# Optimization experiments

Hardware: AMD Instinct MI355X
Metric: run time of the kernel (lower is better)

The kernel has to match this reference:

```python
import jax, jax.numpy as jnp
import numpy as np

INPUT_SIZE = 64
HIDDEN = 128
BATCH = 512
SEQ = 512


def setup_inputs() -> dict:
    key = jax.random.key(0)
    ks = jax.random.split(key, 7)
    s_ih = 1.0 / np.sqrt(HIDDEN)
    token = jax.random.normal(ks[0], (BATCH, SEQ, INPUT_SIZE), dtype=jnp.float32)
    W_ih = jax.random.uniform(ks[1], (HIDDEN, INPUT_SIZE), jnp.float32, -s_ih, s_ih)
    W_hh = jax.random.uniform(ks[2], (HIDDEN, HIDDEN), jnp.float32, -s_ih, s_ih)
    b_ih = jax.random.uniform(ks[3], (HIDDEN,), jnp.float32, -s_ih, s_ih)
    b_hh = jax.random.uniform(ks[4], (HIDDEN,), jnp.float32, -s_ih, s_ih)
    W_lin = jax.random.uniform(ks[5], (1, HIDDEN), jnp.float32, -s_ih, s_ih)
    b_lin = jax.random.uniform(ks[6], (1,), jnp.float32, -s_ih, s_ih)
    return {"token": token, "W_ih": W_ih, "W_hh": W_hh, "b_ih": b_ih,
            "b_hh": b_hh, "W_lin": W_lin, "b_lin": b_lin}


def reference(token, W_ih, W_hh, b_ih, b_hh, W_lin, b_lin):
    # Precompute input projection for all timesteps: [T, B, H]
    x_proj = jnp.einsum('bti,hi->tbh', token, W_ih) + b_ih + b_hh
    h0 = jnp.zeros((token.shape[0], W_hh.shape[0]), dtype=token.dtype)

    def step(h, xp):
        h_new = jnp.tanh(xp + h @ W_hh.T)
        return h_new, None

    h_last, _ = jax.lax.scan(step, h0, x_proj)
    # Linear head on last hidden state: [B, 1]
    return h_last @ W_lin.T + b_lin
```

## Files before the change

kernel.cpp:

```cpp
#include <hip/hip_runtime.h>

#define B_ 512
#define T_ 512
#define I_ 64
#define H_ 128
#define CHUNK 64
#define NCHUNK (T_ / CHUNK)

#define TOKBYTES 16384
#define HB0      (2 * TOKBYTES)
#define HB1      (HB0 + 512)
#define DUMMY    (HB1 + 512)
#define LDS_SZ   (DUMMY + 256)

__device__ __forceinline__ void gload_lds16(const float* g, void* l) {
    __builtin_amdgcn_global_load_lds(
        (const __attribute__((address_space(1))) unsigned int*)g,
        (__attribute__((address_space(3))) unsigned int*)l, 16, 0, 0);
}

#define FM(a, x, w) "v_fmac_f32 v" #a ", v" #x ", v" #w "\n\t"
#define SC(n) "v_mul_f32 v" #n ", 0x4038aa3b, v" #n "\n\t"

#define CLOBS \
    "v48","v49","v50","v51","v52","v53","v54","v55","v56","v57","v58","v59", \
    "v60","v61","v62","v63","v64","v65","v66","v67","v68","v69","v70","v71", \
    "v72","v73","v74","v75","v76","v77","v78","v79","v80","v81","v82","v83", \
    "v84","v85","v86","v87","v88","v89","v90","v91","v92","v93","v94","v95", \
    "v96","v97","v98","v99","v100","v101","v102","v103","v104","v105","v106", \
    "v107","v108","v109","v110","v111","v112","v113","v114","v115","v116", \
    "v117","v118","v119","v120","v121","v122","v123","v124","v125","v126", \
    "v127","memory"

#define RNN_STEP(TOKA, HRD, HWR, BA, BB, PAR)                                 \
    asm volatile(                                                             \
        "ds_read_b128 v[56:59], %0\n\t"                                       \
        "ds_read_b128 v[60:63], %0 offset:128\n\t"                            \
        "ds_read_b128 v[64:67], %1\n\t"                                       \
        "ds_read_b128 v[68:71], %1 offset:128\n\t"                            \
        "ds_read_b128 v[72:75], %1 offset:256\n\t"                            \
        "ds_read_b128 v[76:79], %1 offset:384\n\t"                            \
        "v_add_u32 %0, 256, %0\n\t"                                           \
        "s_waitcnt lgkmcnt(4)\n\t"                                            \
        "v_fma_f32 v48, v56, v112, %3\n\t"                                    \
        "v_mul_f32 v49, v57, v113\n\t"                                        \
        "v_mul_f32 v50, v58, v114\n\t"                                        \
        "v_mul_f32 v51, v59, v115\n\t"                                        \
        "v_fma_f32 v52, v56, v120, %4\n\t"                                    \
        "v_mul_f32 v53, v57, v121\n\t"                                        \
        "v_mul_f32 v54, v58, v122\n\t"                                        \
        "v_mul_f32 v55, v59, v123\n\t"                                        \
        FM(48,60,116) FM(49,61,117) FM(50,62,118) FM(51,63,119)               \
        FM(52,60,124) FM(53,61,125) FM(54,62,126) FM(55,63,127)               \
        "s_waitcnt lgkmcnt(2)\n\t"                                            \
        FM(48,64,80)  FM(49,65,81)  FM(50,66,82)  FM(51,67,83)                \
        FM(52,64,96)  FM(53,65,97)  FM(54,66,98)  FM(55,67,99)                \
        FM(48,68,84)  FM(49,69,85)  FM(50,70,86)  FM(51,71,87)                \
        FM(52,68,100) FM(53,69,101) FM(54,70,102) FM(55,71,103)               \
        "s_waitcnt lgkmcnt(0)\n\t"                                            \
        FM(48,72,88)  FM(49,73,89)  FM(50,74,90)  FM(51,75,91)                \
        FM(52,72,104) FM(53,73,105) FM(54,74,106) FM(55,75,107)               \
        FM(48,76,92)  FM(49,77,93)  FM(50,78,94)  FM(51,79,95)                \
        FM(52,76,108) FM(53,77,109) FM(54,78,110) FM(55,79,111)               \
        "v_add_f32 v48, v48, v49\n\t"                                         \
        "v_add_f32 v50, v50, v51\n\t"                                         \
        "v_add_f32 v52, v52, v53\n\t"                                         \
        "v_add_f32 v54, v54, v55\n\t"                                         \
        "v_add_f32 v48, v48, v50\n\t"                                         \
        "v_add_f32 v52, v52, v54\n\t"                                         \
        "s_nop 1\n\t"                                                         \
        "v_add_f32 v48, v48, v48 quad_perm:[1,0,3,2] row_mask:0xf bank_mask:0xf\n\t" \
        "v_add_f32 v52, v52, v52 quad_perm:[1,0,3,2] row_mask:0xf bank_mask:0xf\n\t" \
        "v_cndmask_b32 v49, v48, v52, %5\n\t"                                 \
        "s_nop 1\n\t"                                                         \
        "v_add_f32 v49, v49, v49 quad_perm:[2,3,0,1] row_mask:0xf bank_mask:0xf\n\t" \
        "s_nop 1\n\t"                                                         \
        "v_add_f32 v49, v49, v49 row_shl:4 row_mask:0xf bank_mask:0x5\n\t"    \
        "s_nop 1\n\t"                                                         \
        "v_exp_f32 v49, v49\n\t"                                              \
        "s_nop 0\n\t"                                                         \
        "v_add_f32 v49, 1.0, v49\n\t"                                         \
        "v_rcp_f32 v50, v49\n\t"                                              \
        "s_nop 0\n\t"                                                         \
        "v_fma_f32 v49, v50, -2.0, 1.0\n\t"                                   \
        "ds_write_b32 %2, v49\n\t"                                            \
        "s_waitcnt lgkmcnt(0)\n\t"                                            \
        "s_barrier"                                                           \
        : "+v"(TOKA)                                                          \
        : "v"(HRD), "v"(HWR), "v"(BA), "v"(BB), "s"(PAR)                      \
        : CLOBS)

__global__ __launch_bounds__(512) __attribute__((amdgpu_waves_per_eu(4, 4)))
void rnn_kernel(const float* __restrict__ token,
                const float* __restrict__ W_ih,
                const float* __restrict__ W_hh,
                const float* __restrict__ b_ih,
                const float* __restrict__ b_hh,
                const float* __restrict__ W_lin,
                const float* __restrict__ b_lin,
                float* __restrict__ out)
{
    __shared__ __align__(16) char lds[LDS_SZ];
    const unsigned lb =
        (unsigned)(uintptr_t)(__attribute__((address_space(3))) char*)lds;

    const int tid = threadIdx.x;
    const int e   = tid & 7;
    const int G   = tid >> 3;
    const int b   = blockIdx.x;
    const int j0  = 2 * G, j1 = 2 * G + 1;

    {
        const float* pA = W_hh + j0 * H_ + e * 16;
        const float* pB = W_hh + j1 * H_ + e * 16;
        const float* pC = W_ih + j0 * I_ + e * 8;
        const float* pD = W_ih + j1 * I_ + e * 8;
        asm volatile(
            "global_load_dwordx4 v[80:83], %0, off\n\t"
            "global_load_dwordx4 v[84:87], %0, off offset:16\n\t"
            "global_load_dwordx4 v[88:91], %0, off offset:32\n\t"
            "global_load_dwordx4 v[92:95], %0, off offset:48\n\t"
            "global_load_dwordx4 v[96:99], %1, off\n\t"
            "global_load_dwordx4 v[100:103], %1, off offset:16\n\t"
            "global_load_dwordx4 v[104:107], %1, off offset:32\n\t"
            "global_load_dwordx4 v[108:111], %1, off offset:48\n\t"
            "global_load_dwordx4 v[112:115], %2, off\n\t"
            "global_load_dwordx4 v[116:119], %2, off offset:16\n\t"
            "global_load_dwordx4 v[120:123], %3, off\n\t"
            "global_load_dwordx4 v[124:127], %3, off offset:16\n\t"
            "s_waitcnt vmcnt(0)\n\t"
            SC(80) SC(81) SC(82) SC(83) SC(84) SC(85) SC(86) SC(87)
            SC(88) SC(89) SC(90) SC(91) SC(92) SC(93) SC(94) SC(95)
            SC(96) SC(97) SC(98) SC(99) SC(100) SC(101) SC(102) SC(103)
            SC(104) SC(105) SC(106) SC(107) SC(108) SC(109) SC(110) SC(111)
            SC(112) SC(113) SC(114) SC(115) SC(116) SC(117) SC(118) SC(119)
            SC(120) SC(121) SC(122) SC(123) SC(124) SC(125) SC(126) SC(127)
            :: "v"(pA), "v"(pB), "v"(pC), "v"(pD) : CLOBS);
    }

    const float biasA = (b_ih[j0] + b_hh[j0]) * (2.885390081777927f / 8.0f);
    const float biasB = (b_ih[j1] + b_hh[j1]) * (2.885390081777927f / 8.0f);
    const unsigned long long par = 0xAAAAAAAAAAAAAAAAULL;

    const int  jsel   = 2 * G + (e & 1);
    const int  wloc   = ((jsel >> 2) & 3) * 32 + (jsel >> 4) * 4 + (jsel & 3);
    const bool writer = (e < 2);
    const unsigned dmy = lb + DUMMY + (tid & 63) * 4;
    const unsigned hw0 = writer ? (lb + HB1 + wloc * 4) : dmy;
    const unsigned hw1 = writer ? (lb + HB0 + wloc * 4) : dmy;
    const unsigned hr0 = lb + HB0 + e * 16;
    const unsigned hr1 = lb + HB1 + e * 16;

    const float* tok_row = token + (size_t)b * T_ * I_;
    const int S0 = tid, S1 = 512 + tid;
    const int so0 = (S0 >> 4) * 64 + (S0 & 7) * 8 + ((S0 >> 3) & 1) * 4;
    const int so1 = (S1 >> 4) * 64 + (S1 & 7) * 8 + ((S1 >> 3) & 1) * 4;

    gload_lds16(tok_row + so0, lds + S0 * 16);
    gload_lds16(tok_row + so1, lds + S1 * 16);
    if (tid < H_) *(float*)(lds + HB0 + tid * 4) = 0.0f;
    asm volatile("s_waitcnt vmcnt(0) lgkmcnt(0)\n\ts_barrier" ::: "memory");

#pragma unroll 1
    for (int c = 0; c < NCHUNK; ++c) {
        const int cb = c & 1;
        const bool has_next = (c + 1 < NCHUNK);
        if (has_next) {
            const float* g = tok_row + (size_t)(c + 1) * CHUNK * I_;
            char* dst = lds + (cb ^ 1) * TOKBYTES;
            gload_lds16(g + so0, dst + S0 * 16);
            gload_lds16(g + so1, dst + S1 * 16);
        }
        unsigned toka = lb + cb * TOKBYTES + e * 16;

#pragma unroll 1
        for (int tt = 0; tt < CHUNK; tt += 2) {
            RNN_STEP(toka, hr0, hw0, biasA, biasB, par);
            RNN_STEP(toka, hr1, hw1, biasA, biasB, par);
        }

        if (has_next) {
            asm volatile("s_waitcnt vmcnt(0)\n\ts_barrier" ::: "memory");
        }
    }

    if (tid < 64) {
        const int a0 = tid, a1 = tid + 64;
        const int l0 = ((a0 >> 2) & 3) * 32 + (a0 >> 4) * 4 + (a0 & 3);
        const int l1 = ((a1 >> 2) & 3) * 32 + (a1 >> 4) * 4 + (a1 & 3);
        float p = *(const float*)(lds + HB0 + l0 * 4) * W_lin[a0]
                + *(const float*)(lds + HB0 + l1 * 4) * W_lin[a1];
#pragma unroll
        for (int off = 32; off; off >>= 1) p += __shfl_down(p, off);
        if (tid == 0) out[b] = p + b_lin[0];
    }
}

extern "C" void kernel_launch(void* const* d_in, const int* in_sizes, int n_in,
                              void* d_out, int out_size, void* d_ws, size_t ws_size,
                              hipStream_t stream) {
    const float* token = (const float*)d_in[0];
    const float* W_ih  = (const float*)d_in[1];
    const float* W_hh  = (const float*)d_in[2];
    const float* b_ih  = (const float*)d_in[3];
    const float* b_hh  = (const float*)d_in[4];
    const float* W_lin = (const float*)d_in[5];
    const float* b_lin = (const float*)d_in[6];
    float* out = (float*)d_out;

    hipLaunchKernelGGL(rnn_kernel, dim3(B_), dim3(512), 0, stream,
                       token, W_ih, W_hh, b_ih, b_hh, W_lin, b_lin, out);
}
```

Measured before the change: 230.3 us.

## Split each hidden row across 16 lanes with 4 rows per group

Work is redistributed so each group of 16 lanes computes 4 hidden units instead of 8 lanes computing 2. Each lane now reads fewer LDS vectors per step (3 b128 instead of 6) and drops the partial-sum add tree, relying on a DPP butterfly with two select masks to merge four outputs. The goal is to shorten the per-step critical path in the serial recurrence. The token and hidden-state LDS layouts and the writer-address mapping change to match, with the risk of a longer cross-lane reduction chain.

```diff
diff --git a/kernel.cpp b/kernel.cpp
--- a/kernel.cpp
+++ b/kernel.cpp
@@ -32,62 +32,58 @@
     "v117","v118","v119","v120","v121","v122","v123","v124","v125","v126", \
     "v127","memory"
 
-#define RNN_STEP(TOKA, HRD, HWR, BA, BB, PAR)                                 \
+#define RNN_STEP(TOKA, HRD, HWR, BA, BB, BC, BD, M1, M2)                      \
     asm volatile(                                                             \
         "ds_read_b128 v[56:59], %0\n\t"                                       \
-        "ds_read_b128 v[60:63], %0 offset:128\n\t"                            \
         "ds_read_b128 v[64:67], %1\n\t"                                       \
-        "ds_read_b128 v[68:71], %1 offset:128\n\t"                            \
-        "ds_read_b128 v[72:75], %1 offset:256\n\t"                            \
-        "ds_read_b128 v[76:79], %1 offset:384\n\t"                            \
+        "ds_read_b128 v[68:71], %1 offset:256\n\t"                            \
         "v_add_u32 %0, 256, %0\n\t"                                           \
-        "s_waitcnt lgkmcnt(4)\n\t"                                            \
+        "s_waitcnt lgkmcnt(2)\n\t"                                            \
         "v_fma_f32 v48, v56, v112, %3\n\t"                                    \
-        "v_mul_f32 v49, v57, v113\n\t"                                        \
-        "v_mul_f32 v50, v58, v114\n\t"                                        \
-        "v_mul_f32 v51, v59, v115\n\t"                                        \
-        "v_fma_f32 v52, v56, v120, %4\n\t"                                    \
-        "v_mul_f32 v53, v57, v121\n\t"                                        \
-        "v_mul_f32 v54, v58, v122\n\t"                                        \
-        "v_mul_f32 v55, v59, v123\n\t"                                        \
-        FM(48,60,116) FM(49,61,117) FM(50,62,118) FM(51,63,119)               \
-        FM(52,60,124) FM(53,61,125) FM(54,62,126) FM(55,63,127)               \
-        "s_waitcnt lgkmcnt(2)\n\t"                                            \
-        FM(48,64,80)  FM(49,65,81)  FM(50,66,82)  FM(51,67,83)                \
-        FM(52,64,96)  FM(53,65,97)  FM(54,66,98)  FM(55,67,99)                \
-        FM(48,68,84)  FM(49,69,85)  FM(50,70,86)  FM(51,71,87)                \
-        FM(52,68,100) FM(53,69,101) FM(54,70,102) FM(55,71,103)               \
+        "v_fma_f32 v49, v56, v116, %4\n\t"                                    \
+        "v_fma_f32 v50, v56, v120, %5\n\t"                                    \
+        "v_fma_f32 v51, v56, v124, %6\n\t"                                    \
+        FM(48,57,113) FM(49,57,117) FM(50,57,121) FM(51,57,125)               \
+        FM(48,58,114) FM(49,58,118) FM(50,58,122) FM(51,58,126)               \
+        FM(48,59,115) FM(49,59,119) FM(50,59,123) FM(51,59,127)               \
+        "s_waitcnt lgkmcnt(1)\n\t"                                            \
+        FM(48,64,80) FM(49,64,88) FM(50,64,96)  FM(51,64,104)                 \
+        FM(48,65,81) FM(49,65,89) FM(50,65,97)  FM(51,65,105)                 \
+        FM(48,66,82) FM(49,66,90) FM(50,66,98)  FM(51,66,106)                 \
+        FM(48,67,83) FM(49,67,91) FM(50,67,99)  FM(51,67,107)                 \
         "s_waitcnt lgkmcnt(0)\n\t"                                            \
-        FM(48,72,88)  FM(49,73,89)  FM(50,74,90)  FM(51,75,91)                \
-        FM(52,72,104) FM(53,73,105) FM(54,74,106) FM(55,75,107)               \
-        FM(48,76,92)  FM(49,77,93)  FM(50,78,94)  FM(51,79,95)                \
-        FM(52,76,108) FM(53,77,109) FM(54,78,110) FM(55,79,111)               \
-        "v_add_f32 v48, v48, v49\n\t"                                         \
-        "v_add_f32 v50, v50, v51\n\t"                                         \
-        "v_add_f32 v52, v52, v53\n\t"                                         \
-        "v_add_f32 v54, v54, v55\n\t"                                         \
-        "v_add_f32 v48, v48, v50\n\t"                                         \
-        "v_add_f32 v52, v52, v54\n\t"                                         \
+        FM(48,68,84) FM(49,68,92) FM(50,68,100) FM(51,68,108)                 \
+        FM(48,69,85) FM(49,69,93) FM(50,69,101) FM(51,69,109)                 \
+        FM(48,70,86) FM(49,70,94) FM(50,70,102) FM(51,70,110)                 \
+        FM(48,71,87) FM(49,71,95) FM(50,71,103) FM(51,71,111)                 \
         "s_nop 1\n\t"                                                         \
         "v_add_f32 v48, v48, v48 quad_perm:[1,0,3,2] row_mask:0xf bank_mask:0xf\n\t" \
-        "v_add_f32 v52, v52, v52 quad_perm:[1,0,3,2] row_mask:0xf bank_mask:0xf\n\t" \
-        "v_cndmask_b32 v49, v48, v52, %5\n\t"                                 \
-        "s_nop 1\n\t"                                                         \
-        "v_add_f32 v49, v49, v49 quad_perm:[2,3,0,1] row_mask:0xf bank_mask:0xf\n\t" \
-        "s_nop 1\n\t"                                                         \
-        "v_add_f32 v49, v49, v49 row_shl:4 row_mask:0xf bank_mask:0x5\n\t"    \
-        "s_nop 1\n\t"                                                         \
-        "v_exp_f32 v49, v49\n\t"                                              \
+        "v_add_f32 v49, v49, v49 quad_perm:[1,0,3,2] row_mask:0xf bank_mask:0xf\n\t" \
+        "v_add_f32 v50, v50, v50 quad_perm:[1,0,3,2] row_mask:0xf bank_mask:0xf\n\t" \
+        "v_add_f32 v51, v51, v51 quad_perm:[1,0,3,2] row_mask:0xf bank_mask:0xf\n\t" \
+        "v_cndmask_b32 v52, v48, v49, %7\n\t"                                 \
+        "v_cndmask_b32 v53, v50, v51, %7\n\t"                                 \
         "s_nop 0\n\t"                                                         \
-        "v_add_f32 v49, 1.0, v49\n\t"                                         \
-        "v_rcp_f32 v50, v49\n\t"                                              \
+        "v_add_f32 v52, v52, v52 quad_perm:[2,3,0,1] row_mask:0xf bank_mask:0xf\n\t" \
+        "v_add_f32 v53, v53, v53 quad_perm:[2,3,0,1] row_mask:0xf bank_mask:0xf\n\t" \
+        "v_cndmask_b32 v54, v52, v53, %8\n\t"                                 \
+        "s_nop 1\n\t"                                                         \
+        "v_add_f32 v54, v54, v54 row_shl:8 row_mask:0xf bank_mask:0x3\n\t"    \
+        "s_nop 1\n\t"                                                         \
+        "v_add_f32 v54, v54, v54 row_shl:4 row_mask:0xf bank_mask:0x1\n\t"    \
+        "s_nop 1\n\t"                                                         \
+        "v_exp_f32 v54, v54\n\t"                                              \
         "s_nop 0\n\t"                                                         \
-        "v_fma_f32 v49, v50, -2.0, 1.0\n\t"                                   \
-        "ds_write_b32 %2, v49\n\t"                                            \
+        "v_add_f32 v54, 1.0, v54\n\t"                                         \
+        "v_rcp_f32 v55, v54\n\t"                                              \
+        "s_nop 0\n\t"                                                         \
+        "v_fma_f32 v54, v55, -2.0, 1.0\n\t"                                   \
+        "ds_write_b32 %2, v54\n\t"                                            \
         "s_waitcnt lgkmcnt(0)\n\t"                                            \
         "s_barrier"                                                           \
         : "+v"(TOKA)                                                          \
-        : "v"(HRD), "v"(HWR), "v"(BA), "v"(BB), "s"(PAR)                      \
+        : "v"(HRD), "v"(HWR), "v"(BA), "v"(BB), "v"(BC), "v"(BD),             \
+          "s"(M1), "s"(M2)                                                    \
         : CLOBS)
 
 __global__ __launch_bounds__(512) __attribute__((amdgpu_waves_per_eu(4, 4)))
@@ -105,29 +101,27 @@
         (unsigned)(uintptr_t)(__attribute__((address_space(3))) char*)lds;
 
     const int tid = threadIdx.x;
-    const int e   = tid & 7;
-    const int G   = tid >> 3;
+    const int e   = tid & 15;
+    const int G   = tid >> 4;
     const int b   = blockIdx.x;
-    const int j0  = 2 * G, j1 = 2 * G + 1;
+    const int jb  = 4 * G;
 
     {
-        const float* pA = W_hh + j0 * H_ + e * 16;
-        const float* pB = W_hh + j1 * H_ + e * 16;
-        const float* pC = W_ih + j0 * I_ + e * 8;
-        const float* pD = W_ih + j1 * I_ + e * 8;
+        const float* pWh = W_hh + jb * H_ + e * 8;
+        const float* pWi = W_ih + jb * I_ + e * 4;
         asm volatile(
-            "global_load_dwordx4 v[80:83], %0, off\n\t"
-            "global_load_dwordx4 v[84:87], %0, off offset:16\n\t"
-            "global_load_dwordx4 v[88:91], %0, off offset:32\n\t"
-            "global_load_dwordx4 v[92:95], %0, off offset:48\n\t"
-            "global_load_dwordx4 v[96:99], %1, off\n\t"
-            "global_load_dwordx4 v[100:103], %1, off offset:16\n\t"
-            "global_load_dwordx4 v[104:107], %1, off offset:32\n\t"
-            "global_load_dwordx4 v[108:111], %1, off offset:48\n\t"
-            "global_load_dwordx4 v[112:115], %2, off\n\t"
-            "global_load_dwordx4 v[116:119], %2, off offset:16\n\t"
-            "global_load_dwordx4 v[120:123], %3, off\n\t"
-            "global_load_dwordx4 v[124:127], %3, off offset:16\n\t"
+            "global_load_dwordx4 v[80:83],   %0, off\n\t"
+            "global_load_dwordx4 v[84:87],   %0, off offset:16\n\t"
+            "global_load_dwordx4 v[88:91],   %0, off offset:512\n\t"
+            "global_load_dwordx4 v[92:95],   %0, off offset:528\n\t"
+            "global_load_dwordx4 v[96:99],   %0, off offset:1024\n\t"
+            "global_load_dwordx4 v[100:103], %0, off offset:1040\n\t"
+            "global_load_dwordx4 v[104:107], %0, off offset:1536\n\t"
+            "global_load_dwordx4 v[108:111], %0, off offset:1552\n\t"
+            "global_load_dwordx4 v[112:115], %1, off\n\t"
+            "global_load_dwordx4 v[116:119], %1, off offset:256\n\t"
+            "global_load_dwordx4 v[120:123], %1, off offset:512\n\t"
+            "global_load_dwordx4 v[124:127], %1, off offset:768\n\t"
             "s_waitcnt vmcnt(0)\n\t"
             SC(80) SC(81) SC(82) SC(83) SC(84) SC(85) SC(86) SC(87)
             SC(88) SC(89) SC(90) SC(91) SC(92) SC(93) SC(94) SC(95)
@@ -135,29 +129,31 @@
             SC(104) SC(105) SC(106) SC(107) SC(108) SC(109) SC(110) SC(111)
             SC(112) SC(113) SC(114) SC(115) SC(116) SC(117) SC(118) SC(119)
             SC(120) SC(121) SC(122) SC(123) SC(124) SC(125) SC(126) SC(127)
-            :: "v"(pA), "v"(pB), "v"(pC), "v"(pD) : CLOBS);
+            :: "v"(pWh), "v"(pWi) : CLOBS);
     }
 
-    const float biasA = (b_ih[j0] + b_hh[j0]) * (2.885390081777927f / 8.0f);
-    const float biasB = (b_ih[j1] + b_hh[j1]) * (2.885390081777927f / 8.0f);
-    const unsigned long long par = 0xAAAAAAAAAAAAAAAAULL;
-
-    const int  jsel   = 2 * G + (e & 1);
-    const int  wloc   = ((jsel >> 2) & 3) * 32 + (jsel >> 4) * 4 + (jsel & 3);
-    const bool writer = (e < 2);
+    const float k16 = 2.885390081777927f / 16.0f;
+    const float biasA = (b_ih[jb + 0] + b_hh[jb + 0]) * k16;
+    const float biasB = (b_ih[jb + 1] + b_hh[jb + 1]) * k16;
+    const float biasC = (b_ih[jb + 2] + b_hh[jb + 2]) * k16;
+    const float biasD = (b_ih[jb + 3] + b_hh[jb + 3]) * k16;
+    const unsigned long long M1 = 0xAAAAAAAAAAAAAAAAULL;
+    const unsigned long long M2 = 0xCCCCCCCCCCCCCCCCULL;
+
+    const int  jsel   = jb + (e & 3);
+    const int  wbyte  = ((((jsel >> 2) & 1) * 16 + (jsel >> 3)) * 16) + (jsel & 3) * 4;
+    const bool writer = (e < 4);
     const unsigned dmy = lb + DUMMY + (tid & 63) * 4;
-    const unsigned hw0 = writer ? (lb + HB1 + wloc * 4) : dmy;
-    const unsigned hw1 = writer ? (lb + HB0 + wloc * 4) : dmy;
+    const unsigned hw0 = writer ? (lb + HB1 + wbyte) : dmy;
+    const unsigned hw1 = writer ? (lb + HB0 + wbyte) : dmy;
     const unsigned hr0 = lb + HB0 + e * 16;
     const unsigned hr1 = lb + HB1 + e * 16;
 
     const float* tok_row = token + (size_t)b * T_ * I_;
     const int S0 = tid, S1 = 512 + tid;
-    const int so0 = (S0 >> 4) * 64 + (S0 & 7) * 8 + ((S0 >> 3) & 1) * 4;
-    const int so1 = (S1 >> 4) * 64 + (S1 & 7) * 8 + ((S1 >> 3) & 1) * 4;
-
-    gload_lds16(tok_row + so0, lds + S0 * 16);
-    gload_lds16(tok_row + so1, lds + S1 * 16);
+
+    gload_lds16(tok_row + S0 * 4, lds + S0 * 16);
+    gload_lds16(tok_row + S1 * 4, lds + S1 * 16);
     if (tid < H_) *(float*)(lds + HB0 + tid * 4) = 0.0f;
     asm volatile("s_waitcnt vmcnt(0) lgkmcnt(0)\n\ts_barrier" ::: "memory");
 
@@ -168,15 +164,15 @@
         if (has_next) {
             const float* g = tok_row + (size_t)(c + 1) * CHUNK * I_;
             char* dst = lds + (cb ^ 1) * TOKBYTES;
-            gload_lds16(g + so0, dst + S0 * 16);
-            gload_lds16(g + so1, dst + S1 * 16);
+            gload_lds16(g + S0 * 4, dst + S0 * 16);
+            gload_lds16(g + S1 * 4, dst + S1 * 16);
         }
         unsigned toka = lb + cb * TOKBYTES + e * 16;
 
 #pragma unroll 1
         for (int tt = 0; tt < CHUNK; tt += 2) {
-            RNN_STEP(toka, hr0, hw0, biasA, biasB, par);
-            RNN_STEP(toka, hr1, hw1, biasA, biasB, par);
+            RNN_STEP(toka, hr0, hw0, biasA, biasB, biasC, biasD, M1, M2);
+            RNN_STEP(toka, hr1, hw1, biasA, biasB, biasC, biasD, M1, M2);
         }
 
         if (has_next) {
@@ -186,8 +182,8 @@
 
     if (tid < 64) {
         const int a0 = tid, a1 = tid + 64;
-        const int l0 = ((a0 >> 2) & 3) * 32 + (a0 >> 4) * 4 + (a0 & 3);
-        const int l1 = ((a1 >> 2) & 3) * 32 + (a1 >> 4) * 4 + (a1 & 3);
+        const int l0 = (((a0 >> 2) & 1) * 16 + (a0 >> 3)) * 4 + (a0 & 3);
+        const int l1 = (((a1 >> 2) & 1) * 16 + (a1 >> 3)) * 4 + (a1 & 3);
         float p = *(const float*)(lds + HB0 + l0 * 4) * W_lin[a0]
                 + *(const float*)(lds + HB0 + l1 * 4) * W_lin[a1];
 #pragma unroll
```

After: 206.8 us. 1.11x faster.
